# Optimization experiments

Hardware: AMD Instinct MI355X
Metric: run time of the kernel (lower is better)

## Reference

```python
import jax, jax.numpy as jnp
import numpy as np

LB = 8      # luma bins
CM = 1      # channel multiplier
GC = 16     # guide complexity
NIN, NOUT = 4, 3
BN_EPS = 1e-5


def bilateral_slice(grid, guide):
    # grid: [B, gh, gw, gd, C]; guide: [B, H, W] in [0,1]
    B, gh, gw, gd, C = grid.shape
    _, H, W = guide.shape
    dt = guide.dtype
    hg = (jnp.arange(H, dtype=dt) + 0.5) * (gh / H) - 0.5   # [H]
    wg = (jnp.arange(W, dtype=dt) + 0.5) * (gw / W) - 0.5   # [W]
    zg = guide * gd - 0.5                                    # [B,H,W]
    h0 = jnp.floor(hg); w0 = jnp.floor(wg); z0 = jnp.floor(zg)
    fh = hg - h0; fw = wg - w0; fz = zg - z0
    h0 = h0.astype(jnp.int32); w0 = w0.astype(jnp.int32); z0 = z0.astype(jnp.int32)
    bidx = jnp.arange(B)[:, None, None]
    out = jnp.zeros((B, H, W, C), dtype=grid.dtype)
    for dh in (0, 1):
        hi = jnp.clip(h0 + dh, 0, gh - 1)          # [H]
        wh_h = fh if dh else (1.0 - fh)
        for dw in (0, 1):
            wi = jnp.clip(w0 + dw, 0, gw - 1)      # [W]
            wh_w = fw if dw else (1.0 - fw)
            w_hw = (wh_h[:, None] * wh_w[None, :])[None]  # [1,H,W]
            for dz in (0, 1):
                zi = jnp.clip(z0 + dz, 0, gd - 1)  # [B,H,W]
                wh_z = fz if dz else (1.0 - fz)
                g = grid[bidx, hi[None, :, None], wi[None, None, :], zi]  # [B,H,W,C]
                out = out + g * (w_hw * wh_z)[..., None]
    return out


def conv1x1(x, w, b):
    # x: [B,Cin,H,W], w: [Cout,Cin], b: [Cout]
    return jnp.einsum('oc,bchw->bohw', w, x) + b[None, :, None, None]


def setup_inputs() -> dict:
    key = jax.random.key(0)
    ks = jax.random.split(key, 12)
    B, H, W, GH, GW = 4, 1024, 1024, 16, 16
    fullres = jax.random.uniform(ks[0], (B, 3, H, W), dtype=jnp.float32)
    local_features = jax.random.normal(ks[1], (B, 8 * CM * LB, GH, GW), dtype=jnp.float32)
    global_features = jax.random.normal(ks[2], (B, 8 * CM * LB), dtype=jnp.float32)
    cout = LB * NOUT * NIN  # 96
    fusion_w = jax.random.normal(ks[3], (cout, 8 * CM * LB), dtype=jnp.float32) * 0.1
    fusion_b = jnp.zeros((cout,), dtype=jnp.float32)
    g1_w = jax.random.normal(ks[4], (GC, 3), dtype=jnp.float32) * 0.5
    g1_b = jnp.zeros((GC,), dtype=jnp.float32)
    bn_gamma = jnp.ones((GC,), dtype=jnp.float32)
    bn_beta = jnp.zeros((GC,), dtype=jnp.float32)
    bn_mean = jnp.zeros((GC,), dtype=jnp.float32)
    bn_var = jnp.ones((GC,), dtype=jnp.float32)
    g2_w = jax.random.normal(ks[5], (1, GC), dtype=jnp.float32) * 0.3
    g2_b = jnp.zeros((1,), dtype=jnp.float32)
    return dict(fullres=fullres, local_features=local_features, global_features=global_features,
                fusion_w=fusion_w, fusion_b=fusion_b, g1_w=g1_w, g1_b=g1_b,
                bn_gamma=bn_gamma, bn_beta=bn_beta, bn_mean=bn_mean, bn_var=bn_var,
                g2_w=g2_w, g2_b=g2_b)


def reference(fullres, local_features, global_features, fusion_w, fusion_b,
              g1_w, g1_b, bn_gamma, bn_beta, bn_mean, bn_var, g2_w, g2_b):
    B = fullres.shape[0]
    # Fusion: relu(local + broadcast global), then 1x1 conv to 96 channels
    fused = jax.nn.relu(local_features + global_features[:, :, None, None])
    x = conv1x1(fused, fusion_w, fusion_b)                    # [B,96,GH,GW]
    GH, GW = x.shape[2], x.shape[3]
    # split(12, dim=1) + stack(dim=2) -> [B,12,LB,GH,GW]
    coeffs = x.reshape(B, LB, NIN * NOUT, GH, GW).transpose(0, 2, 1, 3, 4)
    # GuideNN: 1x1 conv + BN(eval) + relu, then 1x1 conv + sigmoid
    g = conv1x1(fullres, g1_w, g1_b)
    g = (g - bn_mean[None, :, None, None]) * (bn_gamma[None, :, None, None] *
        jax.lax.rsqrt(bn_var + BN_EPS)[None, :, None, None]) + bn_beta[None, :, None, None]
    g = jax.nn.relu(g)
    guide = jax.nn.sigmoid(conv1x1(g, g2_w, g2_b))[:, 0]      # [B,H,W]
    # Slicing: permute grid to [B,GH,GW,LB,12], trilinear slice, back to NCHW
    grid = coeffs.transpose(0, 3, 4, 2, 1)
    sliced = bilateral_slice(grid, guide)                     # [B,H,W,12]
    coeff = sliced.transpose(0, 3, 1, 2)                      # [B,12,H,W]
    # ApplyCoeffs
    R = jnp.sum(fullres * coeff[:, 0:3], axis=1, keepdims=True) + coeff[:, 9:10]
    G = jnp.sum(fullres * coeff[:, 3:6], axis=1, keepdims=True) + coeff[:, 10:11]
    Bc = jnp.sum(fullres * coeff[:, 6:9], axis=1, keepdims=True) + coeff[:, 11:12]
    return jnp.tanh(jnp.concatenate([R, G, Bc], axis=1))
```

## Files before the change

### kernel.cpp

```cpp
#include <hip/hip_runtime.h>
#include <math.h>


#define GRIDBUF_FLOATS (4 * 16 * 16 * 96)
#define CELL_STRIDE 100

typedef float  f4 __attribute__((ext_vector_type(4)));
typedef int    i4 __attribute__((ext_vector_type(4)));
typedef float  f2 __attribute__((ext_vector_type(2)));

__device__ inline f4 splat4(float x) { f4 v = {x, x, x, x}; return v; }
__device__ inline f2 splat2(float x) { f2 v; v.x = x; v.y = x; return v; }

__device__ inline f4 fast_tanh4(f4 x) {
    f4 ax = __builtin_elementwise_abs(x);
    f4 xx = ax * splat4(2.88539008178f);
    f4 e;
    e.x = __builtin_amdgcn_exp2f(xx.x);
    e.y = __builtin_amdgcn_exp2f(xx.y);
    e.z = __builtin_amdgcn_exp2f(xx.z);
    e.w = __builtin_amdgcn_exp2f(xx.w);
    f4 ep1 = e + splat4(1.0f);
    f4 r;
    r.x = __builtin_amdgcn_rcpf(ep1.x);
    r.y = __builtin_amdgcn_rcpf(ep1.y);
    r.z = __builtin_amdgcn_rcpf(ep1.z);
    r.w = __builtin_amdgcn_rcpf(ep1.w);
    f4 t = splat4(1.0f) - (r + r);
    i4 sgn = __builtin_bit_cast(i4, x) &
             (i4){(int)0x80000000, (int)0x80000000, (int)0x80000000, (int)0x80000000};
    return __builtin_bit_cast(f4, __builtin_bit_cast(i4, t) | sgn);
}

__global__ __launch_bounds__(128) void coeff_kernel(
    const float* __restrict__ lf,
    const float* __restrict__ gf,
    const float* __restrict__ fw,
    const float* __restrict__ fb,
    const float* __restrict__ g1w,
    const float* __restrict__ g1b,
    const float* __restrict__ bng,
    const float* __restrict__ bnb,
    const float* __restrict__ bnm,
    const float* __restrict__ bnv,
    const float* __restrict__ g2w,
    const float* __restrict__ g2b,
    float* __restrict__ gridbuf,
    float* __restrict__ params)
{
    __shared__ float fused[64];
    const int blk = blockIdx.x;
    const int b   = blk >> 8;
    const int pos = blk & 255;
    const int t   = threadIdx.x;

    if (t < 64) {
        float v = lf[(b * 64 + t) * 256 + pos] + gf[b * 64 + t];
        fused[t] = v > 0.0f ? v : 0.0f;
    }
    __syncthreads();

    if (t < 96) {
        float acc = fb[t];
        const float* wrow = fw + t * 64;
#pragma unroll
        for (int i = 0; i < 64; ++i) acc = fmaf(wrow[i], fused[i], acc);
        gridbuf[blk * 96 + t] = acc;
    }

    if (blk == 0 && t >= 96 && t < 112) {
        int k = t - 96;
        float a = bng[k] * rsqrtf(bnv[k] + 1e-5f);
        params[k]      = g1w[k * 3 + 0] * a;
        params[16 + k] = g1w[k * 3 + 1] * a;
        params[32 + k] = g1w[k * 3 + 2] * a;
        params[48 + k] = (g1b[k] - bnm[k]) * a + bnb[k];
        params[64 + k] = g2w[k] * 1.44269504f;
        if (k == 0) params[80] = g2b[0] * 1.44269504f;
    }
}

__global__ __launch_bounds__(256) void slice_apply_kernel(
    const float* __restrict__ fullres,
    const float* __restrict__ gridbuf,
    const float* __restrict__ params,
    float* __restrict__ out)
{
    __shared__ __align__(16) float hrow[16 * CELL_STRIDE];

    const int t   = threadIdx.x;
    const int blk = blockIdx.x;
    const int b   = blk >> 10;
    const int y   = blk & 1023;

    const int xb      = t << 2;
    const int pixbase = (y << 10) + xb;
    const int planeB  = (b * 3) << 20;

    f4 rr = *(const f4*)(fullres + planeB + (0 << 20) + pixbase);
    f4 gg = *(const f4*)(fullres + planeB + (1 << 20) + pixbase);
    f4 bb = *(const f4*)(fullres + planeB + (2 << 20) + pixbase);

    {
        const int h0i  = (y < 32) ? -1 : ((y - 32) >> 6);
        const float fh = ((float)y * 0.015625f + (0.0078125f - 0.5f)) - (float)h0i;
        const int hc0  = h0i < 0 ? 0 : h0i;
        const int hc1  = (h0i + 1) > 15 ? 15 : (h0i + 1);
        const float* row0 = gridbuf + (b * 256 + hc0 * 16) * 96;
        const float* row1 = gridbuf + (b * 256 + hc1 * 16) * 96;
        const float wfh0 = 1.0f - fh;

        {
            const int i  = t << 2;
            const int wc = i / 96;
            const int rm = i - wc * 96;
            f4 a = *(const f4*)(row0 + i);
            f4 c = *(const f4*)(row1 + i);
            f4 r = __builtin_elementwise_fma(a, splat4(wfh0), c * splat4(fh));
            *(f4*)(hrow + wc * CELL_STRIDE + rm) = r;
        }
        if (t < 128) {
            const int i  = (t + 256) << 2;
            const int wc = i / 96;
            const int rm = i - wc * 96;
            f4 a = *(const f4*)(row0 + i);
            f4 c = *(const f4*)(row1 + i);
            f4 r = __builtin_elementwise_fma(a, splat4(wfh0), c * splat4(fh));
            *(f4*)(hrow + wc * CELL_STRIDE + rm) = r;
        }
    }
    __syncthreads();

    const int w0i = (xb < 32) ? -1 : ((xb - 32) >> 6);
    const int wc0 = w0i < 0 ? 0 : w0i;
    const int wc1 = (w0i + 1) > 15 ? 15 : (w0i + 1);
    const float fw0 = (float)xb * 0.015625f + (0.0078125f - 0.5f) - (float)w0i;
    const float* cell0 = hrow + wc0 * CELL_STRIDE;
    const float* cell1 = hrow + wc1 * CELL_STRIDE;

    f4 acc = splat4(params[80]);
#pragma unroll
    for (int k = 0; k < 16; ++k) {
        f4 gk = __builtin_elementwise_fma(rr, splat4(params[k]),
                __builtin_elementwise_fma(gg, splat4(params[16 + k]),
                __builtin_elementwise_fma(bb, splat4(params[32 + k]),
                                          splat4(params[48 + k]))));
        gk = __builtin_elementwise_max(gk, splat4(0.0f));
        acc = __builtin_elementwise_fma(gk, splat4(params[64 + k]), acc);
    }
    f4 zg;
    zg.x = fmaf(8.0f, __builtin_amdgcn_rcpf(1.0f + __builtin_amdgcn_exp2f(-acc.x)), -0.5f);
    zg.y = fmaf(8.0f, __builtin_amdgcn_rcpf(1.0f + __builtin_amdgcn_exp2f(-acc.y)), -0.5f);
    zg.z = fmaf(8.0f, __builtin_amdgcn_rcpf(1.0f + __builtin_amdgcn_exp2f(-acc.z)), -0.5f);
    zg.w = fmaf(8.0f, __builtin_amdgcn_rcpf(1.0f + __builtin_amdgcn_exp2f(-acc.w)), -0.5f);

    f4 Rp, Gp, Bp;
#pragma unroll
    for (int px = 0; px < 4; ++px) {
        const float zgp = zg[px];
        int   z0 = (int)floorf(zgp);
        float fz = zgp - (float)z0;
        int zc0 = z0 < 0 ? 0 : z0;
        int zc1 = (z0 + 1) > 7 ? 7 : (z0 + 1);

        const float fw_ = fw0 + (float)px * 0.015625f;
        const float ww0 = 1.0f - fw_;
        const f2 W00 = splat2(ww0 * (1.0f - fz));
        const f2 W01 = splat2(ww0 * fz);
        const f2 W10 = splat2(fw_ * (1.0f - fz));
        const f2 W11 = splat2(fw_ * fz);

        const float4* p00 = (const float4*)(cell0 + zc0 * 12);
        const float4* p01 = (const float4*)(cell0 + zc1 * 12);
        const float4* p10 = (const float4*)(cell1 + zc0 * 12);
        const float4* p11 = (const float4*)(cell1 + zc1 * 12);

        f2 sa[6];
#pragma unroll
        for (int q = 0; q < 3; ++q) {
            float4 a = p00[q], c = p01[q], d = p10[q], e = p11[q];
            f2 alo = (f2){a.x, a.y}, ahi = (f2){a.z, a.w};
            f2 clo = (f2){c.x, c.y}, chi = (f2){c.z, c.w};
            f2 dlo = (f2){d.x, d.y}, dhi = (f2){d.z, d.w};
            f2 elo = (f2){e.x, e.y}, ehi = (f2){e.z, e.w};
            sa[2 * q] =
                __builtin_elementwise_fma(alo, W00,
                __builtin_elementwise_fma(clo, W01,
                __builtin_elementwise_fma(dlo, W10, elo * W11)));
            sa[2 * q + 1] =
                __builtin_elementwise_fma(ahi, W00,
                __builtin_elementwise_fma(chi, W01,
                __builtin_elementwise_fma(dhi, W10, ehi * W11)));
        }

        const float rs = rr[px];
        const float gs = gg[px];
        const float bs = bb[px];
        Rp[px] = fmaf(rs, sa[0].x, fmaf(gs, sa[0].y, fmaf(bs, sa[1].x, sa[4].y)));
        Gp[px] = fmaf(rs, sa[1].y, fmaf(gs, sa[2].x, fmaf(bs, sa[2].y, sa[5].x)));
        Bp[px] = fmaf(rs, sa[3].x, fmaf(gs, sa[3].y, fmaf(bs, sa[4].x, sa[5].y)));
    }

    f4 tR = fast_tanh4(Rp);
    f4 tG = fast_tanh4(Gp);
    f4 tB = fast_tanh4(Bp);

    __builtin_nontemporal_store(tR, (f4*)(out + planeB + (0 << 20) + pixbase));
    __builtin_nontemporal_store(tG, (f4*)(out + planeB + (1 << 20) + pixbase));
    __builtin_nontemporal_store(tB, (f4*)(out + planeB + (2 << 20) + pixbase));
}

extern "C" void kernel_launch(void* const* d_in, const int* in_sizes, int n_in,
                              void* d_out, int out_size, void* d_ws, size_t ws_size,
                              hipStream_t stream) {
    const float* fullres = (const float*)d_in[0];
    const float* lf      = (const float*)d_in[1];
    const float* gf      = (const float*)d_in[2];
    const float* fw      = (const float*)d_in[3];
    const float* fb      = (const float*)d_in[4];
    const float* g1w     = (const float*)d_in[5];
    const float* g1b     = (const float*)d_in[6];
    const float* bng     = (const float*)d_in[7];
    const float* bnb     = (const float*)d_in[8];
    const float* bnm     = (const float*)d_in[9];
    const float* bnv     = (const float*)d_in[10];
    const float* g2w     = (const float*)d_in[11];
    const float* g2b     = (const float*)d_in[12];
    float* out = (float*)d_out;

    float* gridbuf = (float*)d_ws;
    float* params  = gridbuf + GRIDBUF_FLOATS;

    coeff_kernel<<<4 * 256, 128, 0, stream>>>(lf, gf, fw, fb, g1w, g1b,
                                              bng, bnb, bnm, bnv, g2w, g2b,
                                              gridbuf, params);
    slice_apply_kernel<<<4 * 1024, 256, 0, stream>>>(fullres, gridbuf, params, out);
}
```

Baseline: 129.7 us.

## Store h-interpolated grid row in fp16 with padded z-slots in LDS

Converts the per-block interpolated grid row to fp16 in shared memory, padding each z-slice to 16 halves so that two adjacent z levels load as contiguous 16-byte h8 vectors. The z clamping is folded into the weights, using a base index clamped to 0..6 and an adjusted upper weight, which removes separate zc0/zc1 addressing. The aim is to halve LDS footprint and traffic for the slice gather, at the cost of fp16 rounding of the coefficients and extra half-to-float conversions.

```diff
diff --git a/kernel.cpp b/kernel.cpp
--- a/kernel.cpp
+++ b/kernel.cpp
@@ -3,14 +3,15 @@
 
 
 #define GRIDBUF_FLOATS (4 * 16 * 16 * 96)
-#define CELL_STRIDE 100
-
-typedef float  f4 __attribute__((ext_vector_type(4)));
-typedef int    i4 __attribute__((ext_vector_type(4)));
-typedef float  f2 __attribute__((ext_vector_type(2)));
+#define CSH 136
+
+typedef float     f4 __attribute__((ext_vector_type(4)));
+typedef int       i4 __attribute__((ext_vector_type(4)));
+typedef float     f2 __attribute__((ext_vector_type(2)));
+typedef _Float16  h8 __attribute__((ext_vector_type(8)));
+typedef _Float16  h4 __attribute__((ext_vector_type(4)));
 
 __device__ inline f4 splat4(float x) { f4 v = {x, x, x, x}; return v; }
-__device__ inline f2 splat2(float x) { f2 v; v.x = x; v.y = x; return v; }
 
 __device__ inline f4 fast_tanh4(f4 x) {
     f4 ax = __builtin_elementwise_abs(x);
@@ -86,7 +87,7 @@
     const float* __restrict__ params,
     float* __restrict__ out)
 {
-    __shared__ __align__(16) float hrow[16 * CELL_STRIDE];
+    __shared__ __align__(16) _Float16 hrow[16 * CSH];
 
     const int t   = threadIdx.x;
     const int blk = blockIdx.x;
@@ -114,19 +115,23 @@
             const int i  = t << 2;
             const int wc = i / 96;
             const int rm = i - wc * 96;
+            const int z  = rm / 12;
+            const int ch = rm - z * 12;
             f4 a = *(const f4*)(row0 + i);
             f4 c = *(const f4*)(row1 + i);
             f4 r = __builtin_elementwise_fma(a, splat4(wfh0), c * splat4(fh));
-            *(f4*)(hrow + wc * CELL_STRIDE + rm) = r;
+            *(h4*)(hrow + wc * CSH + (z << 4) + ch) = __builtin_convertvector(r, h4);
         }
         if (t < 128) {
             const int i  = (t + 256) << 2;
             const int wc = i / 96;
             const int rm = i - wc * 96;
+            const int z  = rm / 12;
+            const int ch = rm - z * 12;
             f4 a = *(const f4*)(row0 + i);
             f4 c = *(const f4*)(row1 + i);
             f4 r = __builtin_elementwise_fma(a, splat4(wfh0), c * splat4(fh));
-            *(f4*)(hrow + wc * CELL_STRIDE + rm) = r;
+            *(h4*)(hrow + wc * CSH + (z << 4) + ch) = __builtin_convertvector(r, h4);
         }
     }
     __syncthreads();
@@ -135,8 +140,8 @@
     const int wc0 = w0i < 0 ? 0 : w0i;
     const int wc1 = (w0i + 1) > 15 ? 15 : (w0i + 1);
     const float fw0 = (float)xb * 0.015625f + (0.0078125f - 0.5f) - (float)w0i;
-    const float* cell0 = hrow + wc0 * CELL_STRIDE;
-    const float* cell1 = hrow + wc1 * CELL_STRIDE;
+    const _Float16* cell0 = hrow + wc0 * CSH;
+    const _Float16* cell1 = hrow + wc1 * CSH;
 
     f4 acc = splat4(params[80]);
 #pragma unroll
@@ -160,45 +165,46 @@
         const float zgp = zg[px];
         int   z0 = (int)floorf(zgp);
         float fz = zgp - (float)z0;
-        int zc0 = z0 < 0 ? 0 : z0;
-        int zc1 = (z0 + 1) > 7 ? 7 : (z0 + 1);
+        const int   zb   = z0 < 0 ? 0 : (z0 > 6 ? 6 : z0);
+        const float whiz = z0 < 0 ? 0.0f : (z0 > 6 ? 1.0f : fz);
+        const float wloz = 1.0f - whiz;
 
         const float fw_ = fw0 + (float)px * 0.015625f;
         const float ww0 = 1.0f - fw_;
-        const f2 W00 = splat2(ww0 * (1.0f - fz));
-        const f2 W01 = splat2(ww0 * fz);
-        const f2 W10 = splat2(fw_ * (1.0f - fz));
-        const f2 W11 = splat2(fw_ * fz);
-
-        const float4* p00 = (const float4*)(cell0 + zc0 * 12);
-        const float4* p01 = (const float4*)(cell0 + zc1 * 12);
-        const float4* p10 = (const float4*)(cell1 + zc0 * 12);
-        const float4* p11 = (const float4*)(cell1 + zc1 * 12);
-
-        f2 sa[6];
-#pragma unroll
-        for (int q = 0; q < 3; ++q) {
-            float4 a = p00[q], c = p01[q], d = p10[q], e = p11[q];
-            f2 alo = (f2){a.x, a.y}, ahi = (f2){a.z, a.w};
-            f2 clo = (f2){c.x, c.y}, chi = (f2){c.z, c.w};
-            f2 dlo = (f2){d.x, d.y}, dhi = (f2){d.z, d.w};
-            f2 elo = (f2){e.x, e.y}, ehi = (f2){e.z, e.w};
-            sa[2 * q] =
-                __builtin_elementwise_fma(alo, W00,
-                __builtin_elementwise_fma(clo, W01,
-                __builtin_elementwise_fma(dlo, W10, elo * W11)));
-            sa[2 * q + 1] =
-                __builtin_elementwise_fma(ahi, W00,
-                __builtin_elementwise_fma(chi, W01,
-                __builtin_elementwise_fma(dhi, W10, ehi * W11)));
-        }
+        const float W00 = ww0 * wloz;
+        const float W01 = ww0 * whiz;
+        const float W10 = fw_ * wloz;
+        const float W11 = fw_ * whiz;
+
+        const _Float16* c0p = cell0 + (zb << 4);
+        const _Float16* c1p = cell1 + (zb << 4);
+        h8 p000 = *(const h8*)(c0p);
+        h8 p001 = *(const h8*)(c0p + 8);
+        h8 p010 = *(const h8*)(c0p + 16);
+        h8 p011 = *(const h8*)(c0p + 24);
+        h8 p100 = *(const h8*)(c1p);
+        h8 p101 = *(const h8*)(c1p + 8);
+        h8 p110 = *(const h8*)(c1p + 16);
+        h8 p111 = *(const h8*)(c1p + 24);
+
+        float sa[12];
+#pragma unroll
+        for (int ch = 0; ch < 8; ++ch)
+            sa[ch] = fmaf(W00, (float)p000[ch],
+                     fmaf(W01, (float)p010[ch],
+                     fmaf(W10, (float)p100[ch], W11 * (float)p110[ch])));
+#pragma unroll
+        for (int ch = 0; ch < 4; ++ch)
+            sa[8 + ch] = fmaf(W00, (float)p001[ch],
+                         fmaf(W01, (float)p011[ch],
+                         fmaf(W10, (float)p101[ch], W11 * (float)p111[ch])));
 
         const float rs = rr[px];
         const float gs = gg[px];
         const float bs = bb[px];
-        Rp[px] = fmaf(rs, sa[0].x, fmaf(gs, sa[0].y, fmaf(bs, sa[1].x, sa[4].y)));
-        Gp[px] = fmaf(rs, sa[1].y, fmaf(gs, sa[2].x, fmaf(bs, sa[2].y, sa[5].x)));
-        Bp[px] = fmaf(rs, sa[3].x, fmaf(gs, sa[3].y, fmaf(bs, sa[4].x, sa[5].y)));
+        Rp[px] = fmaf(rs, sa[0], fmaf(gs, sa[1], fmaf(bs, sa[2], sa[9])));
+        Gp[px] = fmaf(rs, sa[3], fmaf(gs, sa[4], fmaf(bs, sa[5], sa[10])));
+        Bp[px] = fmaf(rs, sa[6], fmaf(gs, sa[7], fmaf(bs, sa[8], sa[11])));
     }
 
     f4 tR = fast_tanh4(Rp);
```

Result: slower. 140.2 us (+8.1%).
